# Performance work log

Measured on AMD Instinct MI355X. Metric: run time of the kernel, lower is better.

Reference implementation:

```python
import jax, jax.numpy as jnp
import numpy as np

BIG = 1e10  # sentinel for invalid pairwise distances


def get_xyz(depth, fx, fy, cx, cy):
    # depth: [B,1,H,W] -> xyz: [B,3,H,W] via pinhole unprojection
    B, _, H, W = depth.shape
    v = jnp.arange(H, dtype=depth.dtype)[:, None]   # rows
    u = jnp.arange(W, dtype=depth.dtype)[None, :]   # cols
    z = depth[:, 0]                                  # [B,H,W]
    x = (u - cx) / fx * z
    y = (v - cy) / fy * z
    return jnp.stack([x, y, z], axis=1)              # [B,3,H,W]


def _chamfer_item(p, g, vp, vg):
    # p,g: [N,3] point sets; vp,vg: [N] bool validity masks
    # squared pairwise distances via ||p||^2 + ||g||^2 - 2 p.g
    d = (jnp.sum(p * p, -1)[:, None] + jnp.sum(g * g, -1)[None, :]
         - 2.0 * (p @ g.T))                          # [N,N]
    d = jnp.maximum(d, 0.0)
    has_g = jnp.any(vg)
    has_p = jnp.any(vp)
    d1 = jnp.min(jnp.where(vg[None, :], d, BIG), axis=1)  # per pred point
    d2 = jnp.min(jnp.where(vp[:, None], d, BIG), axis=0)  # per gt point
    s1 = jnp.sum(jnp.where(vp & has_g, d1, 0.0))
    s2 = jnp.sum(jnp.where(vg & has_p, d2, 0.0))
    return s1 + s2


def reference(pred, gt_xyz, mask, fx, fy, cx, cy):
    B = pred.shape[0]
    pred_xyz = get_xyz(pred, fx, fy, cx, cy)             # [B,3,H,W]
    p = pred_xyz.reshape(B, 3, -1).transpose(0, 2, 1)    # [B,N,3]
    g = gt_xyz.reshape(B, 3, -1).transpose(0, 2, 1)      # [B,N,3]
    m = mask[:, 0].reshape(B, -1) > 0                    # [B,N]
    # ignore_zeros=True: drop points whose coordinate sum is exactly 0
    vp = m & (jnp.sum(p, -1) != 0)
    vg = m & (jnp.sum(g, -1) != 0)
    per_item = jax.vmap(_chamfer_item)(p, g, vp, vg)     # [B]
    return jnp.sum(per_item) / B


def setup_inputs() -> dict:
    key = jax.random.key(0)
    k1, k2, k3 = jax.random.split(key, 3)
    B, H, W = 2, 128, 128
    pred = jax.random.uniform(k1, (B, 1, H, W), dtype=jnp.float32) * 2.0 + 0.1
    gt_xyz = jax.random.normal(k2, (B, 3, H, W), dtype=jnp.float32)
    mask = jax.random.randint(k3, (B, 1, H, W), 0, 2, dtype=jnp.int32)
    fx = jnp.float32(525.0)
    fy = jnp.float32(525.0)
    cx = jnp.float32(64.0)
    cy = jnp.float32(64.0)
    return {"pred": pred, "gt_xyz": gt_xyz, "mask": mask,
            "fx": fx, "fy": fy, "cx": cx, "cy": cy}
```

## Files before the change

### kernel.cpp

```cpp
#include <hip/hip_runtime.h>

#define B_ITEMS 2
#define W_IMG   128
#define N_PTS   16384
#define CH_GRID 1024
#define SENT    1e18f

__global__ __launch_bounds__(1024) void prep_kernel(
        const float* __restrict__ pred,
        const float* __restrict__ gt,
        const int*   __restrict__ mask,
        const float* fxp, const float* fyp,
        const float* cxp, const float* cyp,
        int*    __restrict__ cnt,
        float4* __restrict__ p4,
        float4* __restrict__ g4,
        float*  __restrict__ out) {
    int s   = blockIdx.x;
    int b   = s & 1;
    int isG = s >> 1;
    int tid = threadIdx.x;
    int lane = tid & 63;

    __shared__ int lcnt;
    if (tid == 0) { lcnt = 0; if (s == 0) out[0] = 0.0f; }
    __syncthreads();

    float4* __restrict__ dst = (isG ? g4 : p4) + b * N_PTS;
    float fx = *fxp, fy = *fyp, cx = *cxp, cy = *cyp;

    for (int iter = 0; iter < N_PTS / 1024; ++iter) {
        int idx = iter * 1024 + tid;
        int mv  = mask[b * N_PTS + idx];
        float x, y, z;
        if (!isG) {
            float u = (float)(idx & (W_IMG - 1));
            float v = (float)(idx >> 7);
            z = pred[b * N_PTS + idx];
            x = (u - cx) / fx * z;
            y = (v - cy) / fy * z;
        } else {
            x = gt[(b * 3 + 0) * N_PTS + idx];
            y = gt[(b * 3 + 1) * N_PTS + idx];
            z = gt[(b * 3 + 2) * N_PTS + idx];
        }
        bool ok = (mv > 0) && (((x + y) + z) != 0.0f);
        unsigned long long bal = __ballot(ok);
        int nw  = __popcll(bal);
        int pre = __popcll(bal & ((1ull << lane) - 1ull));
        int basep = 0;
        if (lane == 0 && nw) basep = atomicAdd(&lcnt, nw);
        basep = __shfl(basep, 0, 64);
        if (ok) dst[basep + pre] = make_float4(x, y, z, 0.0f);
    }
    __syncthreads();

    int c = lcnt;
    int padded = (c + 255) & ~255;
    for (int k = c + tid; k < padded; k += 1024)
        dst[k] = make_float4(SENT, SENT, SENT, 0.0f);
    if (tid == 0) cnt[s] = c;
}

__global__ __launch_bounds__(256, 4) void chamfer_kernel(
        const int*    __restrict__ cnt,
        const float4* __restrict__ p4,
        const float4* __restrict__ g4,
        float* __restrict__ out) {
    int np0 = cnt[0], np1 = cnt[1], ng0 = cnt[2], ng1 = cnt[3];
    int naArr[4] = {np0, ng0, np1, ng1};
    int nbArr[4] = {ng0, np0, ng1, np1};
    const float4* Aarr[4] = {p4, g4, p4 + N_PTS, g4 + N_PTS};
    const float4* Barr[4] = {g4, p4, g4 + N_PTS, p4 + N_PTS};

    int tid = threadIdx.x;
    int tr = tid & 7, tc = tid >> 3;
    __shared__ float smin[4][32];

    int units[4];
    int Utot = 0;
#pragma unroll
    for (int s = 0; s < 4; ++s) {
        units[s] = (naArr[s] > 0 && nbArr[s] > 0) ? ((naArr[s] + 31) >> 5) : 0;
        Utot += units[s];
    }

    for (int u = blockIdx.x; u < Utot; u += CH_GRID) {
        int s = 0, base = 0;
        while (u >= base + units[s]) { base += units[s]; ++s; }
        int chunk = u - base;
        int na = naArr[s], nb = nbArr[s];
        const float4* __restrict__ A  = Aarr[s];
        const float4* __restrict__ Bp = Barr[s];
        int rowbase = chunk * 32;

        float px[4], py[4], pz[4], rm[4];
#pragma unroll
        for (int a = 0; a < 4; ++a) {
            float4 w = A[rowbase + a * 8 + tr];
            px[a] = w.x; py[a] = w.y; pz[a] = w.z;
            rm[a] = 3.4e38f;
        }

        int ntiles = (nb + 255) >> 8;
        float4 bufA[8], bufB[8];
        auto LOADT = [&](float4* buf, int t) {
#pragma unroll
            for (int cb = 0; cb < 8; ++cb)
                buf[cb] = Bp[t * 256 + cb * 32 + tc];
        };
        auto COMPT = [&](const float4* buf) {
#pragma unroll
            for (int cb = 0; cb < 8; ++cb) {
                float gx = buf[cb].x, gy = buf[cb].y, gz = buf[cb].z;
#pragma unroll
                for (int a = 0; a < 4; ++a) {
                    float dx = px[a] - gx;
                    float dy = py[a] - gy;
                    float dz = pz[a] - gz;
                    float d  = fmaf(dx, dx, fmaf(dy, dy, dz * dz));
                    rm[a] = fminf(rm[a], d);
                }
            }
        };

        LOADT(bufA, 0);
        int t = 0;
        while (true) {
            if (t + 1 < ntiles) LOADT(bufB, t + 1);
            COMPT(bufA);
            ++t; if (t >= ntiles) break;
            if (t + 1 < ntiles) LOADT(bufA, t + 1);
            COMPT(bufB);
            ++t; if (t >= ntiles) break;
        }

#pragma unroll
        for (int a = 0; a < 4; ++a) {
            float v = rm[a];
            v = fminf(v, __shfl_xor(v, 8, 64));
            v = fminf(v, __shfl_xor(v, 16, 64));
            v = fminf(v, __shfl_xor(v, 32, 64));
            rm[a] = v;
        }
        int w = tid >> 6;
        if ((tid & 63) < 8) {
#pragma unroll
            for (int a = 0; a < 4; ++a) smin[w][a * 8 + tr] = rm[a];
        }
        __syncthreads();
        if (tid < 32) {
            float v = fminf(fminf(smin[0][tid], smin[1][tid]),
                            fminf(smin[2][tid], smin[3][tid]));
            float contrib = (rowbase + tid < na) ? v : 0.0f;
#pragma unroll
            for (int off = 16; off > 0; off >>= 1)
                contrib += __shfl_down(contrib, off, 32);
            if (tid == 0) atomicAdd(out, contrib * (1.0f / B_ITEMS));
        }
        __syncthreads();
    }
}

extern "C" void kernel_launch(void* const* d_in, const int* in_sizes, int n_in,
                              void* d_out, int out_size, void* d_ws, size_t ws_size,
                              hipStream_t stream) {
    const float* pred = (const float*)d_in[0];
    const float* gt   = (const float*)d_in[1];
    const int*   mask = (const int*)  d_in[2];
    const float* fx   = (const float*)d_in[3];
    const float* fy   = (const float*)d_in[4];
    const float* cx   = (const float*)d_in[5];
    const float* cy   = (const float*)d_in[6];
    float* out = (float*)d_out;

    char* ws = (char*)d_ws;
    int*    cnt = (int*)ws;
    float4* p4  = (float4*)(ws + 256);
    float4* g4  = (float4*)(ws + 256 + (size_t)B_ITEMS * N_PTS * 16);

    prep_kernel<<<dim3(4), 1024, 0, stream>>>(
        pred, gt, mask, fx, fy, cx, cy, cnt, p4, g4, out);

    chamfer_kernel<<<dim3(CH_GRID), 256, 0, stream>>>(cnt, p4, g4, out);
}
```

Baseline: 123.7 us.

## Expand squared distance into dot-product form and widen per-thread row tile

The distance is rewritten as ||b||^2 - 2a·b, so the inner loop needs 3 FMAs plus a min per pair, and ||a||^2 is added after the reduction. Prep now runs on 256 blocks, each compacting its points through a global atomic counter that is zeroed by a memset, and writes both raw and pre-scaled (-2x, ||x||^2) copies. The chamfer kernel handles 64 rows per block with 8 rows per thread and masks a partial tail tile instead of padding with sentinels. The trade-offs are cancellation error in the expanded form, which is clamped with max 0, a point order that is no longer deterministic, and higher register use.

Result: faster. 115.4 us (-6.7%).

```diff
diff --git a/kernel.cpp b/kernel.cpp
--- a/kernel.cpp
+++ b/kernel.cpp
@@ -4,161 +4,181 @@
 #define W_IMG   128
 #define N_PTS   16384
 #define CH_GRID 1024
-#define SENT    1e18f
-
-__global__ __launch_bounds__(1024) void prep_kernel(
+
+__global__ __launch_bounds__(256) void prep_kernel(
         const float* __restrict__ pred,
         const float* __restrict__ gt,
         const int*   __restrict__ mask,
         const float* fxp, const float* fyp,
         const float* cxp, const float* cyp,
         int*    __restrict__ cnt,
-        float4* __restrict__ p4,
-        float4* __restrict__ g4,
+        float4* __restrict__ pR, float4* __restrict__ gR,
+        float4* __restrict__ pT, float4* __restrict__ gT,
         float*  __restrict__ out) {
-    int s   = blockIdx.x;
-    int b   = s & 1;
-    int isG = s >> 1;
-    int tid = threadIdx.x;
-    int lane = tid & 63;
-
-    __shared__ int lcnt;
-    if (tid == 0) { lcnt = 0; if (s == 0) out[0] = 0.0f; }
+    int s    = blockIdx.x >> 6;
+    int b    = s & 1;
+    int isG  = s >> 1;
+    int tid  = threadIdx.x;
+    int idx  = (blockIdx.x & 63) * 256 + tid;
+    int lane = tid & 63, w = tid >> 6;
+
+    if (blockIdx.x == 0 && tid == 0) out[0] = 0.0f;
+
+    float x, y, z;
+    if (!isG) {
+        float fx = *fxp, fy = *fyp, cx = *cxp, cy = *cyp;
+        float u = (float)(idx & (W_IMG - 1));
+        float v = (float)(idx >> 7);
+        z = pred[b * N_PTS + idx];
+        x = (u - cx) / fx * z;
+        y = (v - cy) / fy * z;
+    } else {
+        x = gt[(b * 3 + 0) * N_PTS + idx];
+        y = gt[(b * 3 + 1) * N_PTS + idx];
+        z = gt[(b * 3 + 2) * N_PTS + idx];
+    }
+    int  mv = mask[b * N_PTS + idx];
+    bool ok = (mv > 0) && (((x + y) + z) != 0.0f);
+
+    unsigned long long bal = __ballot(ok);
+    int nw  = __popcll(bal);
+    int pre = __popcll(bal & ((1ull << lane) - 1ull));
+
+    __shared__ int wbase[4];
+    __shared__ int blockbase;
+    if (lane == 0) wbase[w] = nw;
     __syncthreads();
-
-    float4* __restrict__ dst = (isG ? g4 : p4) + b * N_PTS;
-    float fx = *fxp, fy = *fyp, cx = *cxp, cy = *cyp;
-
-    for (int iter = 0; iter < N_PTS / 1024; ++iter) {
-        int idx = iter * 1024 + tid;
-        int mv  = mask[b * N_PTS + idx];
-        float x, y, z;
-        if (!isG) {
-            float u = (float)(idx & (W_IMG - 1));
-            float v = (float)(idx >> 7);
-            z = pred[b * N_PTS + idx];
-            x = (u - cx) / fx * z;
-            y = (v - cy) / fy * z;
-        } else {
-            x = gt[(b * 3 + 0) * N_PTS + idx];
-            y = gt[(b * 3 + 1) * N_PTS + idx];
-            z = gt[(b * 3 + 2) * N_PTS + idx];
-        }
-        bool ok = (mv > 0) && (((x + y) + z) != 0.0f);
-        unsigned long long bal = __ballot(ok);
-        int nw  = __popcll(bal);
-        int pre = __popcll(bal & ((1ull << lane) - 1ull));
-        int basep = 0;
-        if (lane == 0 && nw) basep = atomicAdd(&lcnt, nw);
-        basep = __shfl(basep, 0, 64);
-        if (ok) dst[basep + pre] = make_float4(x, y, z, 0.0f);
+    if (tid == 0) {
+        int s0 = 0;
+#pragma unroll
+        for (int i = 0; i < 4; ++i) { int t = wbase[i]; wbase[i] = s0; s0 += t; }
+        blockbase = s0 ? atomicAdd(&cnt[s], s0) : 0;
     }
     __syncthreads();
 
-    int c = lcnt;
-    int padded = (c + 255) & ~255;
-    for (int k = c + tid; k < padded; k += 1024)
-        dst[k] = make_float4(SENT, SENT, SENT, 0.0f);
-    if (tid == 0) cnt[s] = c;
+    if (ok) {
+        int pos = blockbase + wbase[w] + pre;
+        float ps = fmaf(z, z, fmaf(y, y, x * x));
+        float4* __restrict__ raw = (isG ? gR : pR) + b * N_PTS;
+        float4* __restrict__ tf  = (isG ? gT : pT) + b * N_PTS;
+        raw[pos] = make_float4(x, y, z, ps);
+        tf[pos]  = make_float4(-2.0f * x, -2.0f * y, -2.0f * z, ps);
+    }
 }
 
 __global__ __launch_bounds__(256, 4) void chamfer_kernel(
         const int*    __restrict__ cnt,
-        const float4* __restrict__ p4,
-        const float4* __restrict__ g4,
+        const float4* __restrict__ pR, const float4* __restrict__ gR,
+        const float4* __restrict__ pT, const float4* __restrict__ gT,
         float* __restrict__ out) {
     int np0 = cnt[0], np1 = cnt[1], ng0 = cnt[2], ng1 = cnt[3];
     int naArr[4] = {np0, ng0, np1, ng1};
     int nbArr[4] = {ng0, np0, ng1, np1};
-    const float4* Aarr[4] = {p4, g4, p4 + N_PTS, g4 + N_PTS};
-    const float4* Barr[4] = {g4, p4, g4 + N_PTS, p4 + N_PTS};
+    const float4* Arow[4] = {pR, gR, pR + N_PTS, gR + N_PTS};
+    const float4* Bcol[4] = {gT, pT, gT + N_PTS, pT + N_PTS};
+
+    int units[4];
+    int Utot = 0;
+#pragma unroll
+    for (int i = 0; i < 4; ++i) {
+        units[i] = (naArr[i] > 0 && nbArr[i] > 0) ? ((naArr[i] + 63) >> 6) : 0;
+        Utot += units[i];
+    }
+    int u = blockIdx.x;
+    if (u >= Utot) return;
+    int s = 0;
+    while (u >= units[s]) { u -= units[s]; ++s; }
+    int na = naArr[s], nb = nbArr[s];
+    const float4* __restrict__ A  = Arow[s];
+    const float4* __restrict__ Bp = Bcol[s];
+    int rowbase = u * 64;
 
     int tid = threadIdx.x;
     int tr = tid & 7, tc = tid >> 3;
-    __shared__ float smin[4][32];
-
-    int units[4];
-    int Utot = 0;
-#pragma unroll
-    for (int s = 0; s < 4; ++s) {
-        units[s] = (naArr[s] > 0 && nbArr[s] > 0) ? ((naArr[s] + 31) >> 5) : 0;
-        Utot += units[s];
-    }
-
-    for (int u = blockIdx.x; u < Utot; u += CH_GRID) {
-        int s = 0, base = 0;
-        while (u >= base + units[s]) { base += units[s]; ++s; }
-        int chunk = u - base;
-        int na = naArr[s], nb = nbArr[s];
-        const float4* __restrict__ A  = Aarr[s];
-        const float4* __restrict__ Bp = Barr[s];
-        int rowbase = chunk * 32;
-
-        float px[4], py[4], pz[4], rm[4];
-#pragma unroll
-        for (int a = 0; a < 4; ++a) {
-            float4 w = A[rowbase + a * 8 + tr];
-            px[a] = w.x; py[a] = w.y; pz[a] = w.z;
-            rm[a] = 3.4e38f;
+
+    float px[8], py[8], pz[8], rm[8];
+#pragma unroll
+    for (int a = 0; a < 8; ++a) {
+        float4 v = A[rowbase + a * 8 + tr];
+        px[a] = v.x; py[a] = v.y; pz[a] = v.z;
+        rm[a] = 3.4e38f;
+    }
+
+    int full = nb >> 8;
+    float4 bufA[8], bufB[8];
+    auto LOADT = [&](float4* buf, int t) {
+#pragma unroll
+        for (int cb = 0; cb < 8; ++cb)
+            buf[cb] = Bp[t * 256 + cb * 32 + tc];
+    };
+    auto COMPT = [&](const float4* buf) {
+#pragma unroll
+        for (int cb = 0; cb < 8; ++cb) {
+            float bx = buf[cb].x, by = buf[cb].y, bz = buf[cb].z, bw = buf[cb].w;
+#pragma unroll
+            for (int a = 0; a < 8; ++a) {
+                float t = fmaf(px[a], bx, fmaf(py[a], by, fmaf(pz[a], bz, bw)));
+                rm[a] = fminf(rm[a], t);
+            }
         }
-
-        int ntiles = (nb + 255) >> 8;
-        float4 bufA[8], bufB[8];
-        auto LOADT = [&](float4* buf, int t) {
-#pragma unroll
-            for (int cb = 0; cb < 8; ++cb)
-                buf[cb] = Bp[t * 256 + cb * 32 + tc];
-        };
-        auto COMPT = [&](const float4* buf) {
-#pragma unroll
-            for (int cb = 0; cb < 8; ++cb) {
-                float gx = buf[cb].x, gy = buf[cb].y, gz = buf[cb].z;
-#pragma unroll
-                for (int a = 0; a < 4; ++a) {
-                    float dx = px[a] - gx;
-                    float dy = py[a] - gy;
-                    float dz = pz[a] - gz;
-                    float d  = fmaf(dx, dx, fmaf(dy, dy, dz * dz));
-                    rm[a] = fminf(rm[a], d);
-                }
-            }
-        };
-
+    };
+
+    if (full > 0) {
         LOADT(bufA, 0);
         int t = 0;
-        while (true) {
-            if (t + 1 < ntiles) LOADT(bufB, t + 1);
+        for (; t + 2 <= full; t += 2) {
+            LOADT(bufB, t + 1);
             COMPT(bufA);
-            ++t; if (t >= ntiles) break;
-            if (t + 1 < ntiles) LOADT(bufA, t + 1);
+            if (t + 2 < full) LOADT(bufA, t + 2);
             COMPT(bufB);
-            ++t; if (t >= ntiles) break;
         }
-
-#pragma unroll
-        for (int a = 0; a < 4; ++a) {
-            float v = rm[a];
-            v = fminf(v, __shfl_xor(v, 8, 64));
-            v = fminf(v, __shfl_xor(v, 16, 64));
-            v = fminf(v, __shfl_xor(v, 32, 64));
-            rm[a] = v;
+        if (t < full) COMPT(bufA);
+    }
+
+    if (nb & 255) {
+        int t = full;
+#pragma unroll
+        for (int cb = 0; cb < 8; ++cb) {
+            int j = t * 256 + cb * 32 + tc;
+            float4 v = Bp[j];
+            bool okc = j < nb;
+            float bx = okc ? v.x : 0.0f;
+            float by = okc ? v.y : 0.0f;
+            float bz = okc ? v.z : 0.0f;
+            float bw = okc ? v.w : 3.4e38f;
+#pragma unroll
+            for (int a = 0; a < 8; ++a) {
+                float tv = fmaf(px[a], bx, fmaf(py[a], by, fmaf(pz[a], bz, bw)));
+                rm[a] = fminf(rm[a], tv);
+            }
         }
-        int w = tid >> 6;
-        if ((tid & 63) < 8) {
-#pragma unroll
-            for (int a = 0; a < 4; ++a) smin[w][a * 8 + tr] = rm[a];
-        }
-        __syncthreads();
-        if (tid < 32) {
-            float v = fminf(fminf(smin[0][tid], smin[1][tid]),
-                            fminf(smin[2][tid], smin[3][tid]));
-            float contrib = (rowbase + tid < na) ? v : 0.0f;
-#pragma unroll
-            for (int off = 16; off > 0; off >>= 1)
-                contrib += __shfl_down(contrib, off, 32);
-            if (tid == 0) atomicAdd(out, contrib * (1.0f / B_ITEMS));
-        }
-        __syncthreads();
+    }
+
+#pragma unroll
+    for (int a = 0; a < 8; ++a) {
+        float v = rm[a];
+        v = fminf(v, __shfl_xor(v, 8, 64));
+        v = fminf(v, __shfl_xor(v, 16, 64));
+        v = fminf(v, __shfl_xor(v, 32, 64));
+        rm[a] = v;
+    }
+    __shared__ float smin[4][64];
+    int w = tid >> 6, lane = tid & 63;
+    if (lane < 8) {
+#pragma unroll
+        for (int a = 0; a < 8; ++a) smin[w][a * 8 + lane] = rm[a];
+    }
+    __syncthreads();
+    if (tid < 64) {
+        float v = fminf(fminf(smin[0][tid], smin[1][tid]),
+                        fminf(smin[2][tid], smin[3][tid]));
+        int row = rowbase + tid;
+        float ps = A[row].w;
+        float contrib = (row < na) ? fmaxf(v + ps, 0.0f) : 0.0f;
+#pragma unroll
+        for (int off = 32; off > 0; off >>= 1)
+            contrib += __shfl_down(contrib, off, 64);
+        if (tid == 0) atomicAdd(out, contrib * (1.0f / B_ITEMS));
     }
 }
 
@@ -175,12 +195,18 @@
     float* out = (float*)d_out;
 
     char* ws = (char*)d_ws;
+    size_t SEG = (size_t)B_ITEMS * N_PTS * 16;
     int*    cnt = (int*)ws;
-    float4* p4  = (float4*)(ws + 256);
-    float4* g4  = (float4*)(ws + 256 + (size_t)B_ITEMS * N_PTS * 16);
-
-    prep_kernel<<<dim3(4), 1024, 0, stream>>>(
-        pred, gt, mask, fx, fy, cx, cy, cnt, p4, g4, out);
-
-    chamfer_kernel<<<dim3(CH_GRID), 256, 0, stream>>>(cnt, p4, g4, out);
+    float4* pR  = (float4*)(ws + 256);
+    float4* gR  = (float4*)(ws + 256 + SEG);
+    float4* pT  = (float4*)(ws + 256 + 2 * SEG);
+    float4* gT  = (float4*)(ws + 256 + 3 * SEG);
+
+    hipMemsetAsync(cnt, 0, 16, stream);
+
+    prep_kernel<<<dim3(256), 256, 0, stream>>>(
+        pred, gt, mask, fx, fy, cx, cy, cnt, pR, gR, pT, gT, out);
+
+    chamfer_kernel<<<dim3(CH_GRID), 256, 0, stream>>>(
+        cnt, pR, gR, pT, gT, out);
 }
```
